# Optimization experiments

Hardware: AMD Instinct MI355X
Metric: run time of the kernel (lower is better)

## Reference

```python
import jax, jax.numpy as jnp
import numpy as np

N_ATOMS = 10000
N_PAIRS = 160000
F = 32            # nr_atom_basis (= edge basis = hidden sizes)
H = 7             # nr_heads
C = H * F         # nr_coefficients = 224
N_RBF = 50
RBF_CUTOFF = 5.0
RBF_GAMMA = 10.0

silu = jax.nn.silu

def setup_inputs() -> dict:
    key = jax.random.key(0)
    ks = jax.random.split(key, 32)
    def w(k, shape, scale=0.1):
        return (jax.random.normal(k, shape, dtype=jnp.float32) * scale)
    inp = {
        "h": jax.random.normal(ks[0], (N_ATOMS, F), dtype=jnp.float32),
        "x": jax.random.normal(ks[1], (N_ATOMS, 3), dtype=jnp.float32),
        "v": jax.random.normal(ks[2], (N_ATOMS, 3), dtype=jnp.float32),
        "pairlist": jax.random.randint(ks[3], (2, N_PAIRS), 0, N_ATOMS, dtype=jnp.int64 if jax.config.read('jax_enable_x64') else jnp.int32),
        # edge model (ContinuousFilterConvolutionWithConcatenation)
        "w_mlp_in": w(ks[4], (2 * F, N_RBF)), "b_mlp_in": jnp.zeros((N_RBF,), jnp.float32),
        "w_e1": w(ks[5], (2 * F + N_RBF + 1, F)), "b_e1": jnp.zeros((F,), jnp.float32),
        "w_e2": w(ks[6], (F, F)), "b_e2": jnp.zeros((F,), jnp.float32),
        # semantic attention mlp
        "w_att": w(ks[7], (F, H)), "b_att": jnp.zeros((H,), jnp.float32),
        # node mlp: in = F + C + F
        "w_n1": w(ks[8], (F + C + F, F)), "b_n1": jnp.zeros((F,), jnp.float32),
        "w_n2": w(ks[9], (F, F)), "b_n2": jnp.zeros((F,), jnp.float32),
        # post norm mlp
        "w_p1": w(ks[10], (C, F)), "b_p1": jnp.zeros((F,), jnp.float32),
        "w_p2": w(ks[11], (F, F)), "b_p2": jnp.zeros((F,), jnp.float32),
        # velocity mlp
        "w_v1": w(ks[12], (F, F)), "b_v1": jnp.zeros((F,), jnp.float32),
        "w_v2": w(ks[13], (F, 1)),
        # mixers
        "w_xmix": w(ks[14], (C, C)),
        "w_vmix": w(ks[15], (C, 1)),
    }
    return inp

def _rbf(d):  # Gaussian smearing, [P] -> [P, N_RBF]
    centers = jnp.linspace(0.0, RBF_CUTOFF, N_RBF, dtype=jnp.float32)
    return jnp.exp(-RBF_GAMMA * (d[:, None] - centers) ** 2)

def reference(h, x, v, pairlist,
              w_mlp_in, b_mlp_in, w_e1, b_e1, w_e2, b_e2,
              w_att, b_att, w_n1, b_n1, w_n2, b_n2,
              w_p1, b_p1, w_p2, b_p2, w_v1, b_v1, w_v2,
              w_xmix, w_vmix):
    n = h.shape[0]
    p = pairlist.shape[1]
    idx_i, idx_j = pairlist[0], pairlist[1]

    r_ij = x[idx_j] - x[idx_i]                       # [P, 3]
    d_ij = jnp.linalg.norm(r_ij, axis=-1)            # [P]
    dir_ij = r_ij / (d_ij[:, None] + 1e-5)           # [P, 3]

    # edge model
    h_cat = jnp.concatenate([h[idx_i], h[idx_j]], axis=-1)         # [P, 2F]
    filt = _rbf(d_ij) * (h_cat @ w_mlp_in + b_mlp_in)              # [P, N_RBF]
    e_in = jnp.concatenate([h_cat, filt, d_ij[:, None]], axis=-1)  # [P, 2F+N_RBF+1]
    h_ij_edge = silu(e_in @ w_e1 + b_e1) @ w_e2 + b_e2             # [P, F]

    # semantic attention: scatter-softmax over edges grouped by idx_i
    logits = jax.nn.celu(h_ij_edge @ w_att + b_att, alpha=2.0)     # [P, H]
    seg_max = jax.ops.segment_max(logits, idx_i, num_segments=n)
    e = jnp.exp(logits - seg_max[idx_i])
    seg_sum = jax.ops.segment_sum(e, idx_i, num_segments=n)
    att = e / seg_sum[idx_i]                                       # [P, H]
    att_agg = jax.ops.segment_sum(att, idx_i, num_segments=n)
    att_normed = att / att_agg[idx_i]
    # einsum('pf,ph->pfh') then reshape to [P, C]
    h_ij_semantic = (h_ij_edge[:, :, None] * att_normed[:, None, :]).reshape(p, C)

    # aggregate (scatter_add)
    h_i_semantic = jax.ops.segment_sum(h_ij_semantic, idx_i, num_segments=n)  # [N, C]

    # spatial attention
    x_mixed = jnp.tanh(h_ij_semantic @ w_xmix)                     # [P, C]
    combinations = dir_ij[:, None, :] * x_mixed[:, :, None]        # [P, C, 3]
    counts = jax.ops.segment_sum(jnp.ones((p,), h.dtype), idx_i, num_segments=n)
    denom = jnp.maximum(counts, 1.0)
    comb_mean = jax.ops.segment_sum(combinations, idx_i, num_segments=n) / denom[:, None, None]
    norm_sq = jnp.sum(comb_mean ** 2, axis=-1)                     # [N, C]
    h_i_spatial = silu(silu(norm_sq @ w_p1 + b_p1) @ w_p2 + b_p2)  # [N, F]

    # node update
    node_in = jnp.concatenate([h, h_i_semantic, h_i_spatial], axis=-1)
    h_updated = h + silu(silu(node_in @ w_n1 + b_n1) @ w_n2 + b_n2)

    # velocity update
    v_ij = jnp.einsum('pcx,c->px', combinations, w_vmix[:, 0])     # [P, 3]
    dv = jax.ops.segment_sum(v_ij, idx_i, num_segments=n) / denom[:, None]
    scale = 2.0 * jax.nn.sigmoid(silu(h @ w_v1 + b_v1) @ w_v2)     # [N, 1]
    v_updated = scale * v + dv
    x_updated = x + v_updated
    return (h_updated, x_updated, v_updated)
```

## Files before the change

kernel.cpp:

```cpp
#include <hip/hip_runtime.h>

typedef unsigned short u16;
typedef unsigned int u32;
typedef __attribute__((ext_vector_type(8))) short short8;
typedef __attribute__((ext_vector_type(4))) float floatx4;

#define P_PAIRS 160000
#define N_ATOMS 10000

#define OFF_WMLP  0
#define OFF_BMLP  3200
#define OFF_WE1   3250
#define OFF_BE1   6930
#define OFF_WE2   6962
#define OFF_BE2   7986
#define OFF_WATT  8018
#define OFF_BATT  8242
#define OFF_WN1   8249
#define OFF_BN1   17465
#define OFF_WN2   17497
#define OFF_BN2   18521
#define OFF_WP1   18553
#define OFF_BP1   25721
#define OFF_WP2   25753
#define OFF_BP2   26777
#define OFF_WV1   26809
#define OFF_BV1   27833
#define OFF_WV2   27865
#define OFF_WVMIX 27897
#define WF_TOTAL  28121

__device__ __forceinline__ float b2f(u16 u){ return __uint_as_float(((u32)u) << 16); }
__device__ __forceinline__ u16 f2b(float f){
  u32 u = __float_as_uint(f);
  u32 r = (u + 0x7FFFu + ((u >> 16) & 1u)) >> 16;
  return (u16)r;
}
__device__ __forceinline__ void unpack2(u32 p, float& lo, float& hi){
  lo = __uint_as_float(p << 16);
  hi = __uint_as_float(p & 0xFFFF0000u);
}
__device__ __forceinline__ float siluf(float v){ return v / (1.f + __expf(-v)); }
__device__ __forceinline__ float ldw(const void* p, int o, int bf){
  return bf ? b2f(((const u16*)p)[o]) : ((const float*)p)[o];
}

__global__ void k_code(float* out, float code){
  if (threadIdx.x == 0 && blockIdx.x == 0) out[0] = code;
}

__device__ __forceinline__ void detect_flags(const u32* hw, const u32* plw, int* s_fl){
  int tid = threadIdx.x;
  if (tid < 64){
    u32 e = (hw[tid] >> 7) & 0xFFu;
    unsigned long long m1 = __ballot(e >= 100u && e <= 140u);
    unsigned long long m2 = __ballot(plw[2*tid+1] == 0u);
    if (tid == 0){
      s_fl[0] = (__popcll(m1) >= 48) ? 1 : 0;
      s_fl[1] = (__popcll(m2) >= 60) ? 1 : 0;
    }
  }
  __syncthreads();
}

#define NBP_NORM 2735
#define NBP_CONV (NBP_NORM + 110)
#define NBP_TRAN (NBP_CONV + 196)
#define NBP_PB   (NBP_TRAN + 14)
#define NBP_HIST (NBP_PB + 625)

__global__ void k_prep(const void* __restrict__ h_raw, const void* __restrict__ x_raw,
    const void* __restrict__ v_raw, const void* __restrict__ pl_raw,
    const void* w_mlp, const void* b_mlp, const void* w_e1, const void* b_e1,
    const void* w_e2, const void* b_e2, const void* w_att, const void* b_att,
    const void* w_n1, const void* b_n1, const void* w_n2, const void* b_n2,
    const void* w_p1, const void* b_p1, const void* w_p2, const void* b_p2,
    const void* w_v1, const void* b_v1, const void* w_v2, const void* w_vmix,
    const void* wx,
    float* __restrict__ hf, float* __restrict__ xf, float* __restrict__ vf,
    int* __restrict__ pli, float* __restrict__ Wf, u16* __restrict__ wT,
    u16* __restrict__ bpk, int* __restrict__ counts){
  __shared__ int s_fl[2];
  detect_flags((const u32*)h_raw, (const u32*)pl_raw, s_fl);
  int bf = s_fl[0], i64 = s_fl[1];
  int bid = blockIdx.x, tid = threadIdx.x;
  if (bid < NBP_NORM){
    int t = bid * 256 + tid;
    if (t < 320000){
      hf[t] = ldw(h_raw, t, bf);
    } else if (t < 350000){
      int i = t - 320000; xf[i] = ldw(x_raw, i, bf);
    } else if (t < 380000){
      int i = t - 350000; vf[i] = ldw(v_raw, i, bf);
    } else if (t < 700000){
      int k = t - 380000;
      const int* p32 = (const int*)pl_raw;
      pli[k] = i64 ? p32[2*(size_t)k] : p32[k];
    }
  } else if (bid < NBP_CONV){
    int t = (bid - NBP_NORM) * 256 + tid;
    if (t >= WF_TOTAL) return;
    if (t < 3200){
      int k = t / 50, o = t - k * 50;
      Wf[OFF_WMLP + o * 64 + k] = ldw(w_mlp, t, bf);
      return;
    }
    const void* src; int o;
    if      (t < 3250)  { src = b_mlp;  o = t - 3200; }
    else if (t < 6930)  { src = w_e1;   o = t - 3250; }
    else if (t < 6962)  { src = b_e1;   o = t - 6930; }
    else if (t < 7986)  { src = w_e2;   o = t - 6962; }
    else if (t < 8018)  { src = b_e2;   o = t - 7986; }
    else if (t < 8242)  { src = w_att;  o = t - 8018; }
    else if (t < 8249)  { src = b_att;  o = t - 8242; }
    else if (t < 17465) { src = w_n1;   o = t - 8249; }
    else if (t < 17497) { src = b_n1;   o = t - 17465; }
    else if (t < 18521) { src = w_n2;   o = t - 17497; }
    else if (t < 18553) { src = b_n2;   o = t - 18521; }
    else if (t < 25721) { src = w_p1;   o = t - 18553; }
    else if (t < 25753) { src = b_p1;   o = t - 25721; }
    else if (t < 26777) { src = w_p2;   o = t - 25753; }
    else if (t < 26809) { src = b_p2;   o = t - 26777; }
    else if (t < 27833) { src = w_v1;   o = t - 26809; }
    else if (t < 27865) { src = b_v1;   o = t - 27833; }
    else if (t < 27897) { src = w_v2;   o = t - 27865; }
    else                { src = w_vmix; o = t - 27897; }
    Wf[t] = ldw(src, o, bf);
  } else if (bid < NBP_TRAN){
    int t = (bid - NBP_CONV) * 256 + tid;
    if (t >= 224 * 224) return;
    int n = t / 224, k = t - n * 224;
    wT[t] = f2b(ldw(wx, k * 224 + n, bf));
  } else if (bid < NBP_PB){
    int t = (bid - NBP_TRAN) * 256 + tid;
    if (t >= 3584) return;
    float v = 0.f;
    if (t < 2048){
      int n = t >> 6, k = t & 63;
      if (k < 50)       v = ldw(w_e1, (64 + k) * 32 + n, bf);
      else if (k == 50) v = ldw(w_e1, 114 * 32 + n, bf);
    } else if (t < 3072){
      int e = t - 2048; int n = e >> 5, k = e & 31;
      v = ldw(w_e2, k * 32 + n, bf);
    } else {
      int e = t - 3072; int n = e >> 5, k = e & 31;
      if (n < 7) v = ldw(w_att, k * 7 + n, bf);
    }
    bpk[t] = f2b(v);
  } else {
    int p = (bid - NBP_PB) * 256 + tid;
    const int* p32 = (const int*)pl_raw;
    int i = i64 ? p32[2*(size_t)p] : p32[p];
    atomicAdd(&counts[i], 1);
  }
}

__global__ void k_atomscan(const float* __restrict__ hf, const float* __restrict__ Wf,
    u16* __restrict__ prei, u16* __restrict__ prej,
    const int* __restrict__ counts, int* __restrict__ offs, int* __restrict__ cursor){
  __shared__ float hs[16][33];
  __shared__ int part[256];
  int tid = threadIdx.x;
  if (blockIdx.x < 625){
    int a0 = blockIdx.x * 16;
    for (int e = tid; e < 512; e += 256){
      int a = e >> 5, k = e & 31;
      hs[a][k] = hf[(size_t)(a0 + a) * 32 + k];
    }
    __syncthreads();
    for (int e = tid; e < 800; e += 256){
      int a = e / 50, r = e - a * 50;
      const float* wm = Wf + OFF_WMLP + r * 64;
      float acc = Wf[OFF_BMLP + r];
      #pragma unroll
      for (int k = 0; k < 32; ++k) acc += hs[a][k] * wm[k];
      prei[(size_t)(a0 + a) * 88 + 32 + r] = f2b(acc);
    }
    for (int e = tid; e < 800; e += 256){
      int a = e / 50, r = e - a * 50;
      const float* wm = Wf + OFF_WMLP + r * 64 + 32;
      float acc = 0.f;
      #pragma unroll
      for (int k = 0; k < 32; ++k) acc += hs[a][k] * wm[k];
      prej[(size_t)(a0 + a) * 88 + 32 + r] = f2b(acc);
    }
    for (int e = tid; e < 512; e += 256){
      int a = e >> 5, o = e & 31;
      float acc = Wf[OFF_BE1 + o];
      #pragma unroll
      for (int k = 0; k < 32; ++k) acc += hs[a][k] * Wf[OFF_WE1 + k * 32 + o];
      prei[(size_t)(a0 + a) * 88 + o] = f2b(acc);
    }
    for (int e = tid; e < 512; e += 256){
      int a = e >> 5, o = e & 31;
      float acc = 0.f;
      #pragma unroll
      for (int k = 0; k < 32; ++k) acc += hs[a][k] * Wf[OFF_WE1 + (32 + k) * 32 + o];
      prej[(size_t)(a0 + a) * 88 + o] = f2b(acc);
    }
  } else {
    int sum = 0;
    for (int k = 0; k < 40; ++k){
      int idx = tid * 40 + k;
      if (idx < N_ATOMS) sum += counts[idx];
    }
    part[tid] = sum;
    __syncthreads();
    if (tid == 0){
      int run = 0;
      for (int q = 0; q < 256; ++q){ int tmp = part[q]; part[q] = run; run += tmp; }
    }
    __syncthreads();
    int run = part[tid];
    for (int k = 0; k < 40; ++k){
      int idx = tid * 40 + k;
      if (idx < N_ATOMS){ offs[idx] = run; cursor[idx] = run; run += counts[idx]; }
    }
    if (tid == 0) offs[N_ATOMS] = P_PAIRS;
  }
}

__global__ void k_scatter(const int* __restrict__ pl, int* __restrict__ cursor,
                          int* __restrict__ isrt, int* __restrict__ jsrt){
  int p = blockIdx.x * 256 + threadIdx.x;
  int i = pl[p];
  int pos = atomicAdd(&cursor[i], 1);
  isrt[pos] = i;
  jsrt[pos] = pl[P_PAIRS + p];
}

#define PM_UB   0
#define PM_TB   16384
#define PM_DD   30720
#define PM_A1   31232
#define PM_B1   49664
#define PM_A2   54272
#define PM_B2   64512
#define PM_B3   67072
#define PM_TOT  68352

__global__ __launch_bounds__(256) void k_pairm(const float* __restrict__ x,
    const float* __restrict__ Wf, const u16* __restrict__ prei, const u16* __restrict__ prej,
    const int* __restrict__ isrt, const int* __restrict__ jsrt, const u16* __restrict__ bpk,
    u16* __restrict__ edge, float* __restrict__ logits, float* __restrict__ dirs){
  __shared__ __attribute__((aligned(16))) char smem[PM_TOT];
  float* UB = (float*)(smem + PM_UB);
  u16*   TB = (u16*)(smem + PM_TB);
  float* DD = (float*)(smem + PM_DD);
  u16*   A1 = (u16*)(smem + PM_A1);
  u16*   B1 = (u16*)(smem + PM_B1);
  u16*   A2 = (u16*)(smem + PM_A2);
  u16*   B2 = (u16*)(smem + PM_B2);
  u16*   B3 = (u16*)(smem + PM_B3);
  int tid = threadIdx.x;
  int wave = tid >> 6, lane = tid & 63, l15 = lane & 15, quad = lane >> 4;
  int row0 = blockIdx.x * 128;

  if (tid < 128){
    int s = row0 + tid;
    int i = isrt[s], j = jsrt[s];
    float r0 = x[j*3+0] - x[i*3+0];
    float r1 = x[j*3+1] - x[i*3+1];
    float r2 = x[j*3+2] - x[i*3+2];
    float d = sqrtf(r0*r0 + r1*r1 + r2*r2);
    float rinv = 1.f / (d + 1e-5f);
    dirs[s*3+0] = r0*rinv; dirs[s*3+1] = r1*rinv; dirs[s*3+2] = r2*rinv;
    DD[tid] = d;
    const uint4* pi4 = (const uint4*)(prei + (size_t)i * 88);
    const uint4* pj4 = (const uint4*)(prej + (size_t)j * 88);
    float* ub = UB + tid * 32;
    #pragma unroll
    for (int q = 0; q < 4; ++q){
      uint4 a4 = pi4[q], b4 = pj4[q];
      u32 pa[4] = {a4.x, a4.y, a4.z, a4.w};
      u32 pb[4] = {b4.x, b4.y, b4.z, b4.w};
      #pragma unroll
      for (int w2 = 0; w2 < 4; ++w2){
        float al, ah, bl, bh;
        unpack2(pa[w2], al, ah); unpack2(pb[w2], bl, bh);
        ub[q*8 + w2*2]     = al + bl;
        ub[q*8 + w2*2 + 1] = ah + bh;
      }
    }
    u32* tb = (u32*)TB + tid * 28;
    #pragma unroll
    for (int q = 0; q < 7; ++q){
      uint4 a4 = pi4[4+q], b4 = pj4[4+q];
      u32 pa[4] = {a4.x, a4.y, a4.z, a4.w};
      u32 pb[4] = {b4.x, b4.y, b4.z, b4.w};
      #pragma unroll
      for (int w2 = 0; w2 < 4; ++w2){
        float al, ah, bl, bh;
        unpack2(pa[w2], al, ah); unpack2(pb[w2], bl, bh);
        tb[q*4 + w2] = (u32)f2b(al + bl) | ((u32)f2b(ah + bh) << 16);
      }
    }
  } else {
    int t2 = tid - 128;
    const u32* src = (const u32*)bpk;
    for (int e = t2; e < 1024; e += 128){
      int n = e >> 5, kp = e & 31;
      ((u32*)B1)[n*36 + kp] = src[e];
    }
    for (int e = t2; e < 512; e += 128){
      int n = e >> 4, kp = e & 15;
      ((u32*)B2)[n*20 + kp] = src[1024 + e];
    }
    for (int e = t2; e < 256; e += 128){
      int n = e >> 4, kp = e & 15;
      ((u32*)B3)[n*20 + kp] = src[1536 + e];
    }
  }
  __syncthreads();
  for (int e = tid; e < 4096; e += 256){
    int r = e >> 5, kp = e & 31;
    int k0 = kp * 2, k1 = k0 + 1;
    float d = DD[r];
    float v0 = 0.f, v1 = 0.f;
    if (k0 < 50){
      float t0 = b2f(TB[r*56 + k0]);
      float c0 = (float)k0 * (5.f/49.f), dd0 = d - c0;
      v0 = t0 * __expf(-10.f * dd0 * dd0);
    } else if (k0 == 50) v0 = d;
    if (k1 < 50){
      float t1 = b2f(TB[r*56 + k1]);
      float c1 = (float)k1 * (5.f/49.f), dd1 = d - c1;
      v1 = t1 * __expf(-10.f * dd1 * dd1);
    }
    ((u32*)A1)[r*36 + kp] = (u32)f2b(v0) | ((u32)f2b(v1) << 16);
  }
  __syncthreads();
  floatx4 au[2][2];
  #pragma unroll
  for (int mt = 0; mt < 2; ++mt)
    #pragma unroll
    for (int nt = 0; nt < 2; ++nt) au[mt][nt] = (floatx4){0.f,0.f,0.f,0.f};
  #pragma unroll
  for (int ks = 0; ks < 2; ++ks){
    int kk = ks * 32;
    short8 a0 = *(const short8*)(A1 + (wave*32 + l15)*72 + kk + quad*8);
    short8 a1 = *(const short8*)(A1 + (wave*32 + 16 + l15)*72 + kk + quad*8);
    #pragma unroll
    for (int nt = 0; nt < 2; ++nt){
      short8 b = *(const short8*)(B1 + (nt*16 + l15)*72 + kk + quad*8);
      au[0][nt] = __builtin_amdgcn_mfma_f32_16x16x32_bf16(a0, b, au[0][nt], 0, 0, 0);
      au[1][nt] = __builtin_amdgcn_mfma_f32_16x16x32_bf16(a1, b, au[1][nt], 0, 0, 0);
    }
  }
  #pragma unroll
  for (int mt = 0; mt < 2; ++mt)
    #pragma unroll
    for (int nt = 0; nt < 2; ++nt)
      #pragma unroll
      for (int reg = 0; reg < 4; ++reg){
        int r = wave*32 + mt*16 + quad*4 + reg;
        int c = nt*16 + l15;
        float uval = au[mt][nt][reg] + UB[r*32 + c];
        A2[r*40 + c] = f2b(siluf(uval));
      }
  __syncthreads();
  floatx4 ae[2][2];
  #pragma unroll
  for (int mt = 0; mt < 2; ++mt)
    #pragma unroll
    for (int nt = 0; nt < 2; ++nt) ae[mt][nt] = (floatx4){0.f,0.f,0.f,0.f};
  {
    short8 a0 = *(const short8*)(A2 + (wave*32 + l15)*40 + quad*8);
    short8 a1 = *(const short8*)(A2 + (wave*32 + 16 + l15)*40 + quad*8);
    #pragma unroll
    for (int nt = 0; nt < 2; ++nt){
      short8 b = *(const short8*)(B2 + (nt*16 + l15)*40 + quad*8);
      ae[0][nt] = __builtin_amdgcn_mfma_f32_16x16x32_bf16(a0, b, ae[0][nt], 0, 0, 0);
      ae[1][nt] = __builtin_amdgcn_mfma_f32_16x16x32_bf16(a1, b, ae[1][nt], 0, 0, 0);
    }
  }
  __syncthreads();
  #pragma unroll
  for (int mt = 0; mt < 2; ++mt)
    #pragma unroll
    for (int nt = 0; nt < 2; ++nt)
      #pragma unroll
      for (int reg = 0; reg < 4; ++reg){
        int r = wave*32 + mt*16 + quad*4 + reg;
        int c = nt*16 + l15;
        float ev = ae[mt][nt][reg] + Wf[OFF_BE2 + c];
        A2[r*40 + c] = f2b(ev);
      }
  __syncthreads();
  {
    int r = tid >> 1, p = tid & 1;
    const uint4* srcp = (const uint4*)(A2 + r*40 + p*16);
    uint4* dstp = (uint4*)(edge + (size_t)(row0 + r)*32 + p*16);
    dstp[0] = srcp[0]; dstp[1] = srcp[1];
  }
  floatx4 al_[2];
  al_[0] = (floatx4){0.f,0.f,0.f,0.f};
  al_[1] = (floatx4){0.f,0.f,0.f,0.f};
  {
    short8 a0 = *(const short8*)(A2 + (wave*32 + l15)*40 + quad*8);
    short8 a1 = *(const short8*)(A2 + (wave*32 + 16 + l15)*40 + quad*8);
    short8 b = *(const short8*)(B3 + l15*40 + quad*8);
    al_[0] = __builtin_amdgcn_mfma_f32_16x16x32_bf16(a0, b, al_[0], 0, 0, 0);
    al_[1] = __builtin_amdgcn_mfma_f32_16x16x32_bf16(a1, b, al_[1], 0, 0, 0);
  }
  if (l15 < 7){
    float ba = Wf[OFF_BATT + l15];
    #pragma unroll
    for (int mt = 0; mt < 2; ++mt)
      #pragma unroll
      for (int reg = 0; reg < 4; ++reg){
        int r = wave*32 + mt*16 + quad*4 + reg;
        float vv = al_[mt][reg] + ba;
        float cl = vv > 0.f ? vv : 2.f * expm1f(0.5f * vv);
        logits[(size_t)(row0 + r)*7 + l15] = cl;
      }
  }
}

__global__ __launch_bounds__(256) void k_att(const int* __restrict__ offs,
    const float* __restrict__ logits, const u16* __restrict__ edge,
    float* __restrict__ atts, float* __restrict__ hsem){
  int a = blockIdx.x * 16 + (threadIdx.x >> 4);
  int lane = threadIdx.x & 15;
  int off = offs[a], end = offs[a+1];
  float m[7];
  #pragma unroll
  for (int hh = 0; hh < 7; ++hh) m[hh] = -1e30f;
  for (int s = off + lane; s < end; s += 16){
    #pragma unroll
    for (int hh = 0; hh < 7; ++hh) m[hh] = fmaxf(m[hh], logits[s*7+hh]);
  }
  #pragma unroll
  for (int hh = 0; hh < 7; ++hh){
    float v = m[hh];
    #pragma unroll
    for (int msk = 8; msk >= 1; msk >>= 1) v = fmaxf(v, __shfl_xor(v, msk));
    m[hh] = v;
  }
  float sm[7] = {0,0,0,0,0,0,0};
  for (int s = off + lane; s < end; s += 16){
    #pragma unroll
    for (int hh = 0; hh < 7; ++hh){
      float e = __expf(logits[s*7+hh] - m[hh]);
      sm[hh] += e;
      atts[s*7+hh] = e;
    }
  }
  #pragma unroll
  for (int hh = 0; hh < 7; ++hh){
    float v = sm[hh];
    #pragma unroll
    for (int msk = 8; msk >= 1; msk >>= 1) v += __shfl_xor(v, msk);
    sm[hh] = 1.f / v;
  }
  for (int s = off + lane; s < end; s += 16){
    #pragma unroll
    for (int hh = 0; hh < 7; ++hh) atts[s*7+hh] *= sm[hh];
  }
  __syncthreads();
  float acc[14] = {0,0,0,0,0,0,0,0,0,0,0,0,0,0};
  for (int s = off; s < end; ++s){
    u32 ev = *(const u32*)(edge + (size_t)s * 32 + lane * 2);
    float e0 = b2f((u16)(ev & 0xFFFFu));
    float e1 = b2f((u16)(ev >> 16));
    const float* ap = atts + (size_t)s * 7;
    #pragma unroll
    for (int hh = 0; hh < 7; ++hh){
      float at = ap[hh];
      acc[hh]     += e0 * at;
      acc[7 + hh] += e1 * at;
    }
  }
  float* hp = hsem + (size_t)a * 224 + lane * 14;
  #pragma unroll
  for (int jj = 0; jj < 14; ++jj) hp[jj] = acc[jj];
}

#define GW_EL   29696
#define GW_AL   (29696 + 4608)
#define GW_TOT  36096

__global__ __launch_bounds__(256, 4) void k_gemm3w(const u16* __restrict__ edge,
    const float* __restrict__ atts, const u16* __restrict__ BT,
    u16* __restrict__ xh0, u16* __restrict__ xh1){
  __shared__ __attribute__((aligned(16))) char smem[GW_TOT];
  u16*   As  = (u16*)smem;
  u16*   xth = (u16*)smem;
  u16*   eL  = (u16*)(smem + GW_EL);
  float* aL  = (float*)(smem + GW_AL);
  int tid = threadIdx.x;
  int wave = tid >> 6, lane = tid & 63, l15 = lane & 15, quad = lane >> 4;
  int row0 = blockIdx.x * 64;

  for (int e = tid; e < 512; e += 256){
    int r = e >> 3, q = e & 7;
    *(uint2*)(eL + r*36 + q*4) = *(const uint2*)(edge + (size_t)(row0 + r)*32 + q*4);
  }
  for (int e = tid; e < 448; e += 256) aL[e] = atts[(size_t)row0*7 + e];
  floatx4 acc[14];
  #pragma unroll
  for (int nt = 0; nt < 14; ++nt) acc[nt] = (floatx4){0.f, 0.f, 0.f, 0.f};
  __syncthreads();

  {
    int pr = tid >> 2, q = tid & 3;
    u32* asw = (u32*)As + pr*116 + q*28;
    const u16* er = eL + pr*36 + q*8;
    const float* ar = aL + pr*7;
    float av[7];
    #pragma unroll
    for (int hh = 0; hh < 7; ++hh) av[hh] = ar[hh];
    #pragma unroll
    for (int fo2 = 0; fo2 < 4; ++fo2){
      float e0 = b2f(er[2*fo2]);
      float e1 = b2f(er[2*fo2+1]);
      u16 w[14];
      #pragma unroll
      for (int hh = 0; hh < 7; ++hh){
        w[hh]   = f2b(e0 * av[hh]);
        w[7+hh] = f2b(e1 * av[hh]);
      }
      #pragma unroll
      for (int k = 0; k < 7; ++k)
        asw[fo2*7 + k] = (u32)w[2*k] | ((u32)w[2*k+1] << 16);
    }
  }
  __syncthreads();

  const u16* btbase = BT + (size_t)l15 * 224 + quad * 8;
  for (int kt = 0; kt < 7; ++kt){
    short8 a0 = *(const short8*)(As + (wave*16 + l15)*232 + kt*32 + quad*8);
    const u16* bt = btbase + kt*32;
    #pragma unroll
    for (int nt = 0; nt < 14; ++nt){
      short8 b = *(const short8*)(bt + (size_t)nt*16*224);
      acc[nt] = __builtin_amdgcn_mfma_f32_16x16x32_bf16(a0, b, acc[nt], 0, 0, 0);
    }
  }
  __syncthreads();

  #pragma unroll
  for (int nt = 0; nt < 14; ++nt)
    #pragma unroll
    for (int reg = 0; reg < 4; ++reg){
      int r = wave*16 + quad*4 + reg;
      int c = nt*16 + l15;
      float vv = acc[nt][reg];
      vv = fminf(fmaxf(vv, -15.f), 15.f);
      float e2 = __expf(2.f * vv);
      xth[r*232 + c] = f2b((e2 - 1.f) / (e2 + 1.f));
    }
  __syncthreads();
  for (int e = tid; e < 1792; e += 256){
    int r = e / 28, w = e - r * 28;
    uint4 val = *(const uint4*)(xth + r*232 + w*8);
    if (w < 14) *(uint4*)(xh0 + (size_t)(row0 + r)*112 + w*8) = val;
    else        *(uint4*)(xh1 + (size_t)(row0 + r)*112 + (w-14)*8) = val;
  }
}

#define G_BS   29696
#define G_EL   29696
#define G_AL   (29696 + 4608)
#define G_TOT  38656

__global__ __launch_bounds__(256, 4) void k_gemm3(const u16* __restrict__ edge,
    const float* __restrict__ atts, const u16* __restrict__ BT,
    u16* __restrict__ xhalf, int half){
  __shared__ __attribute__((aligned(16))) char smem[G_TOT];
  u16*   As  = (u16*)smem;
  u16*   xth = (u16*)smem;
  u16*   Bs  = (u16*)(smem + G_BS);
  u16*   eL  = (u16*)(smem + G_EL);
  float* aL  = (float*)(smem + G_AL);
  int tid = threadIdx.x;
  int wave = tid >> 6, lane = tid & 63, l15 = lane & 15, quad = lane >> 4;
  int row0 = blockIdx.x * 64;
  int nbase = half * 112;

  for (int e = tid; e < 512; e += 256){
    int r = e >> 3, q = e & 7;
    *(uint2*)(eL + r*36 + q*4) = *(const uint2*)(edge + (size_t)(row0 + r)*32 + q*4);
  }
  for (int e = tid; e < 448; e += 256) aL[e] = atts[(size_t)row0*7 + e];
  floatx4 acc[7];
  #pragma unroll
  for (int nt = 0; nt < 7; ++nt) acc[nt] = (floatx4){0.f, 0.f, 0.f, 0.f};
  __syncthreads();

  {
    int pr = tid >> 2, q = tid & 3;
    u32* asw = (u32*)As + pr*116 + q*28;
    const u16* er = eL + pr*36 + q*8;
    const float* ar = aL + pr*7;
    float av[7];
    #pragma unroll
    for (int hh = 0; hh < 7; ++hh) av[hh] = ar[hh];
    #pragma unroll
    for (int fo2 = 0; fo2 < 4; ++fo2){
      float e0 = b2f(er[2*fo2]);
      float e1 = b2f(er[2*fo2+1]);
      u16 w[14];
      #pragma unroll
      for (int hh = 0; hh < 7; ++hh){
        w[hh]   = f2b(e0 * av[hh]);
        w[7+hh] = f2b(e1 * av[hh]);
      }
      #pragma unroll
      for (int k = 0; k < 7; ++k)
        asw[fo2*7 + k] = (u32)w[2*k] | ((u32)w[2*k+1] << 16);
    }
  }
  __syncthreads();

  for (int kt = 0; kt < 7; ++kt){
    for (int e = tid; e < 448; e += 256){
      int r = e >> 2, q = e & 3;
      *(uint4*)(Bs + r*40 + q*8) = *(const uint4*)(BT + (size_t)(nbase + r)*224 + kt*32 + q*8);
    }
    __syncthreads();
    int kk = kt * 32;
    short8 a0 = *(const short8*)(As + (wave*16 + l15)*232 + kk + quad*8);
    #pragma unroll
    for (int nt = 0; nt < 7; ++nt){
      short8 b = *(const short8*)(Bs + (nt*16 + l15)*40 + quad*8);
      acc[nt] = __builtin_amdgcn_mfma_f32_16x16x32_bf16(a0, b, acc[nt], 0, 0, 0);
    }
    __syncthreads();
  }

  #pragma unroll
  for (int nt = 0; nt < 7; ++nt)
    #pragma unroll
    for (int reg = 0; reg < 4; ++reg){
      int r = wave*16 + quad*4 + reg;
      int c = nt*16 + l15;
      float vv = acc[nt][reg];
      vv = fminf(fmaxf(vv, -15.f), 15.f);
      float e2 = __expf(2.f * vv);
      xth[r*120 + c] = f2b((e2 - 1.f) / (e2 + 1.f));
    }
  __syncthreads();
  for (int e = tid; e < 896; e += 256){
    int r = e / 14, w = e - r * 14;
    *(uint4*)(xhalf + (size_t)(row0 + r)*112 + w*8) = *(const uint4*)(xth + r*120 + w*8);
  }
}

__global__ __launch_bounds__(256) void k_comb(const int* __restrict__ offs,
    const u16* __restrict__ xhalf, const float* __restrict__ dirs,
    const float* __restrict__ Wf, int half,
    float* __restrict__ nsq, float* __restrict__ pvh){
  int a = blockIdx.x * 16 + (threadIdx.x >> 4);
  int lane = threadIdx.x & 15;
  int off = offs[a], end = offs[a+1];
  float c0[7] = {0,0,0,0,0,0,0}, c1[7] = {0,0,0,0,0,0,0}, c2[7] = {0,0,0,0,0,0,0};
  for (int s = off; s < end; ++s){
    float d0 = dirs[s*3+0], d1 = dirs[s*3+1], d2 = dirs[s*3+2];
    const u16* xr = xhalf + (size_t)s * 112 + lane;
    #pragma unroll
    for (int k = 0; k < 7; ++k){
      float xm = b2f(xr[k*16]);
      c0[k] += d0 * xm; c1[k] += d1 * xm; c2[k] += d2 * xm;
    }
  }
  float inv = 1.f / fmaxf((float)(end - off), 1.f);
  float pv0 = 0.f, pv1 = 0.f, pv2 = 0.f;
  #pragma unroll
  for (int k = 0; k < 7; ++k){
    float m0 = c0[k]*inv, m1 = c1[k]*inv, m2 = c2[k]*inv;
    int c = half*112 + k*16 + lane;
    nsq[(size_t)a*224 + c] = m0*m0 + m1*m1 + m2*m2;
    float wv = Wf[OFF_WVMIX + c];
    pv0 += wv*m0; pv1 += wv*m1; pv2 += wv*m2;
  }
  #pragma unroll
  for (int m = 8; m >= 1; m >>= 1){
    pv0 += __shfl_xor(pv0, m); pv1 += __shfl_xor(pv1, m); pv2 += __shfl_xor(pv2, m);
  }
  if (lane == 0){
    float* pp = pvh + (size_t)half*30000 + (size_t)a*3;
    pp[0] = pv0; pp[1] = pv1; pp[2] = pv2;
  }
}

__global__ __launch_bounds__(256) void k_final4(const float* __restrict__ h,
    const float* __restrict__ x, const float* __restrict__ v,
    const float* __restrict__ Wf, const float* __restrict__ hsem,
    const float* __restrict__ nsq, const float* __restrict__ pvh,
    float* __restrict__ out){
  __shared__ float s_nsq[16][225];
  __shared__ float s_in[16][289];
  __shared__ float s_u1[16][33];
  __shared__ float s_un[16][33];
  __shared__ float s_sc[16];
  int tid = threadIdx.x;
  int a0 = blockIdx.x * 16;
  for (int e = tid; e < 896; e += 256){
    int a = e / 56, q = e - a * 56;
    float4 t = *(const float4*)(nsq + (size_t)(a0 + a) * 224 + q * 4);
    s_nsq[a][q*4+0] = t.x; s_nsq[a][q*4+1] = t.y;
    s_nsq[a][q*4+2] = t.z; s_nsq[a][q*4+3] = t.w;
  }
  for (int e = tid; e < 896; e += 256){
    int a = e / 56, q = e - a * 56;
    float4 t = *(const float4*)(hsem + (size_t)(a0 + a) * 224 + q * 4);
    s_in[a][32 + q*4+0] = t.x; s_in[a][32 + q*4+1] = t.y;
    s_in[a][32 + q*4+2] = t.z; s_in[a][32 + q*4+3] = t.w;
  }
  for (int e = tid; e < 128; e += 256){
    int a = e >> 3, q = e & 7;
    float4 t = *(const float4*)(h + (size_t)(a0 + a) * 32 + q * 4);
    s_in[a][q*4+0] = t.x; s_in[a][q*4+1] = t.y;
    s_in[a][q*4+2] = t.z; s_in[a][q*4+3] = t.w;
  }
  __syncthreads();
  int o = tid & 31, g5 = tid >> 5;
  int aA = g5, aB = g5 + 8;
  {
    float uA = Wf[OFF_BP1 + o], uB = uA;
    const float* w = Wf + OFF_WP1 + o;
    #pragma unroll 8
    for (int kk = 0; kk < 224; ++kk){
      float wv = w[kk*32];
      uA += s_nsq[aA][kk] * wv;
      uB += s_nsq[aB][kk] * wv;
    }
    s_u1[aA][o] = siluf(uA);
    s_u1[aB][o] = siluf(uB);
  }
  {
    float gA = Wf[OFF_BV1 + o], gB = gA;
    const float* w = Wf + OFF_WV1 + o;
    #pragma unroll
    for (int kk = 0; kk < 32; ++kk){
      float wv = w[kk*32];
      gA += s_in[aA][kk] * wv;
      gB += s_in[aB][kk] * wv;
    }
    float wv2 = Wf[OFF_WV2 + o];
    float zA = siluf(gA) * wv2, zB = siluf(gB) * wv2;
    #pragma unroll
    for (int m = 16; m >= 1; m >>= 1){
      zA += __shfl_xor(zA, m); zB += __shfl_xor(zB, m);
    }
    if (o == 0){
      s_sc[aA] = 2.f / (1.f + __expf(-zA));
      s_sc[aB] = 2.f / (1.f + __expf(-zB));
    }
  }
  __syncthreads();
  {
    float uA = Wf[OFF_BP2 + o], uB = uA;
    const float* w = Wf + OFF_WP2 + o;
    #pragma unroll
    for (int kk = 0; kk < 32; ++kk){
      float wv = w[kk*32];
      uA += s_u1[aA][kk] * wv;
      uB += s_u1[aB][kk] * wv;
    }
    s_in[aA][256 + o] = siluf(uA);
    s_in[aB][256 + o] = siluf(uB);
  }
  __syncthreads();
  {
    float uA = Wf[OFF_BN1 + o], uB = uA;
    const float* w = Wf + OFF_WN1 + o;
    #pragma unroll 8
    for (int kk = 0; kk < 288; ++kk){
      float wv = w[kk*32];
      uA += s_in[aA][kk] * wv;
      uB += s_in[aB][kk] * wv;
    }
    s_un[aA][o] = siluf(uA);
    s_un[aB][o] = siluf(uB);
  }
  __syncthreads();
  {
    float uA = Wf[OFF_BN2 + o], uB = uA;
    const float* w = Wf + OFF_WN2 + o;
    #pragma unroll
    for (int kk = 0; kk < 32; ++kk){
      float wv = w[kk*32];
      uA += s_un[aA][kk] * wv;
      uB += s_un[aB][kk] * wv;
    }
    out[(size_t)(a0 + aA)*32 + o] = s_in[aA][o] + siluf(uA);
    out[(size_t)(a0 + aB)*32 + o] = s_in[aB][o] + siluf(uB);
  }
  if (tid < 48){
    int a = tid / 3, c = tid - a * 3;
    int ga = a0 + a;
    float pv = pvh[(size_t)ga*3 + c] + pvh[30000 + (size_t)ga*3 + c];
    float vup = s_sc[a] * v[ga*3 + c] + pv;
    float xup = x[ga*3 + c] + vup;
    out[N_ATOMS*32 + (size_t)ga*3 + c] = xup;
    out[N_ATOMS*32 + N_ATOMS*3 + (size_t)ga*3 + c] = vup;
  }
}

__global__ __launch_bounds__(256) void k_combf(const int* __restrict__ offs,
    const u16* __restrict__ xh0, const u16* __restrict__ xh1,
    const float* __restrict__ dirs, const float* __restrict__ h,
    const float* __restrict__ x, const float* __restrict__ v,
    const float* __restrict__ Wf, const float* __restrict__ hsem,
    float* __restrict__ out){
  __shared__ float s_nsq[16][225];
  __shared__ float s_in[16][289];
  __shared__ float s_u1[16][33];
  __shared__ float s_un[16][33];
  __shared__ float s_sc[16];
  __shared__ float s_pv[16][3];
  int tid = threadIdx.x;
  int a0 = blockIdx.x * 16;
  for (int e = tid; e < 896; e += 256){
    int a = e / 56, q = e - a * 56;
    float4 t = *(const float4*)(hsem + (size_t)(a0 + a) * 224 + q * 4);
    s_in[a][32 + q*4+0] = t.x; s_in[a][32 + q*4+1] = t.y;
    s_in[a][32 + q*4+2] = t.z; s_in[a][32 + q*4+3] = t.w;
  }
  for (int e = tid; e < 128; e += 256){
    int a = e >> 3, q = e & 7;
    float4 t = *(const float4*)(h + (size_t)(a0 + a) * 32 + q * 4);
    s_in[a][q*4+0] = t.x; s_in[a][q*4+1] = t.y;
    s_in[a][q*4+2] = t.z; s_in[a][q*4+3] = t.w;
  }
  {
    int a = tid >> 4, lane = tid & 15;
    int off = offs[a0 + a], end = offs[a0 + a + 1];
    float c0A[7] = {0,0,0,0,0,0,0}, c1A[7] = {0,0,0,0,0,0,0}, c2A[7] = {0,0,0,0,0,0,0};
    float c0B[7] = {0,0,0,0,0,0,0}, c1B[7] = {0,0,0,0,0,0,0}, c2B[7] = {0,0,0,0,0,0,0};
    for (int s = off; s < end; ++s){
      float d0 = dirs[s*3+0], d1 = dirs[s*3+1], d2 = dirs[s*3+2];
      const u16* xra = xh0 + (size_t)s * 112 + lane;
      const u16* xrb = xh1 + (size_t)s * 112 + lane;
      #pragma unroll
      for (int k = 0; k < 7; ++k){
        float xa = b2f(xra[k*16]);
        float xb = b2f(xrb[k*16]);
        c0A[k] += d0 * xa; c1A[k] += d1 * xa; c2A[k] += d2 * xa;
        c0B[k] += d0 * xb; c1B[k] += d1 * xb; c2B[k] += d2 * xb;
      }
    }
    float inv = 1.f / fmaxf((float)(end - off), 1.f);
    float pv0 = 0.f, pv1 = 0.f, pv2 = 0.f;
    #pragma unroll
    for (int k = 0; k < 7; ++k){
      {
        float m0 = c0A[k]*inv, m1 = c1A[k]*inv, m2 = c2A[k]*inv;
        int c = k*16 + lane;
        s_nsq[a][c] = m0*m0 + m1*m1 + m2*m2;
        float wv = Wf[OFF_WVMIX + c];
        pv0 += wv*m0; pv1 += wv*m1; pv2 += wv*m2;
      }
      {
        float m0 = c0B[k]*inv, m1 = c1B[k]*inv, m2 = c2B[k]*inv;
        int c = 112 + k*16 + lane;
        s_nsq[a][c] = m0*m0 + m1*m1 + m2*m2;
        float wv = Wf[OFF_WVMIX + c];
        pv0 += wv*m0; pv1 += wv*m1; pv2 += wv*m2;
      }
    }
    #pragma unroll
    for (int m = 8; m >= 1; m >>= 1){
      pv0 += __shfl_xor(pv0, m); pv1 += __shfl_xor(pv1, m); pv2 += __shfl_xor(pv2, m);
    }
    if (lane == 0){ s_pv[a][0] = pv0; s_pv[a][1] = pv1; s_pv[a][2] = pv2; }
  }
  __syncthreads();
  int o = tid & 31, g5 = tid >> 5;
  int aA = g5, aB = g5 + 8;
  {
    float uA = Wf[OFF_BP1 + o], uB = uA;
    const float* w = Wf + OFF_WP1 + o;
    #pragma unroll 8
    for (int kk = 0; kk < 224; ++kk){
      float wv = w[kk*32];
      uA += s_nsq[aA][kk] * wv;
      uB += s_nsq[aB][kk] * wv;
    }
    s_u1[aA][o] = siluf(uA);
    s_u1[aB][o] = siluf(uB);
  }
  {
    float gA = Wf[OFF_BV1 + o], gB = gA;
    const float* w = Wf + OFF_WV1 + o;
    #pragma unroll
    for (int kk = 0; kk < 32; ++kk){
      float wv = w[kk*32];
      gA += s_in[aA][kk] * wv;
      gB += s_in[aB][kk] * wv;
    }
    float wv2 = Wf[OFF_WV2 + o];
    float zA = siluf(gA) * wv2, zB = siluf(gB) * wv2;
    #pragma unroll
    for (int m = 16; m >= 1; m >>= 1){
      zA += __shfl_xor(zA, m); zB += __shfl_xor(zB, m);
    }
    if (o == 0){
      s_sc[aA] = 2.f / (1.f + __expf(-zA));
      s_sc[aB] = 2.f / (1.f + __expf(-zB));
    }
  }
  __syncthreads();
  {
    float uA = Wf[OFF_BP2 + o], uB = uA;
    const float* w = Wf + OFF_WP2 + o;
    #pragma unroll
    for (int kk = 0; kk < 32; ++kk){
      float wv = w[kk*32];
      uA += s_u1[aA][kk] * wv;
      uB += s_u1[aB][kk] * wv;
    }
    s_in[aA][256 + o] = siluf(uA);
    s_in[aB][256 + o] = siluf(uB);
  }
  __syncthreads();
  {
    float uA = Wf[OFF_BN1 + o], uB = uA;
    const float* w = Wf + OFF_WN1 + o;
    #pragma unroll 8
    for (int kk = 0; kk < 288; ++kk){
      float wv = w[kk*32];
      uA += s_in[aA][kk] * wv;
      uB += s_in[aB][kk] * wv;
    }
    s_un[aA][o] = siluf(uA);
    s_un[aB][o] = siluf(uB);
  }
  __syncthreads();
  {
    float uA = Wf[OFF_BN2 + o], uB = uA;
    const float* w = Wf + OFF_WN2 + o;
    #pragma unroll
    for (int kk = 0; kk < 32; ++kk){
      float wv = w[kk*32];
      uA += s_un[aA][kk] * wv;
      uB += s_un[aB][kk] * wv;
    }
    out[(size_t)(a0 + aA)*32 + o] = s_in[aA][o] + siluf(uA);
    out[(size_t)(a0 + aB)*32 + o] = s_in[aB][o] + siluf(uB);
  }
  if (tid < 48){
    int a = tid / 3, c = tid - a * 3;
    int ga = a0 + a;
    float vup = s_sc[a] * v[ga*3 + c] + s_pv[a][c];
    float xup = x[ga*3 + c] + vup;
    out[N_ATOMS*32 + (size_t)ga*3 + c] = xup;
    out[N_ATOMS*32 + N_ATOMS*3 + (size_t)ga*3 + c] = vup;
  }
}

static constexpr size_t al256(size_t x){ return (x + 255) & ~(size_t)255; }
static constexpr size_t WS_FLAGS   = 0;
static constexpr size_t WS_COUNTS  = al256(WS_FLAGS + 8);
static constexpr size_t WS_OFFSETS = al256(WS_COUNTS + (size_t)N_ATOMS * 4);
static constexpr size_t WS_CURSOR  = al256(WS_OFFSETS + (size_t)(N_ATOMS + 1) * 4);
static constexpr size_t WS_PERM    = al256(WS_CURSOR + (size_t)N_ATOMS * 4);
static constexpr size_t WS_PLI     = al256(WS_PERM + (size_t)P_PAIRS * 4);
static constexpr size_t WS_HF      = al256(WS_PLI + (size_t)2 * P_PAIRS * 4);
static constexpr size_t WS_XF      = al256(WS_HF + (size_t)N_ATOMS * 32 * 4);
static constexpr size_t WS_VF      = al256(WS_XF + (size_t)N_ATOMS * 3 * 4);
static constexpr size_t WS_WF      = al256(WS_VF + (size_t)N_ATOMS * 3 * 4);
static constexpr size_t WS_WT      = al256(WS_WF + (size_t)WF_TOTAL * 4);
static constexpr size_t WS_EDGE    = al256(WS_WT + (size_t)224 * 224 * 2);
static constexpr size_t WS_ATTS    = al256(WS_EDGE + (size_t)P_PAIRS * 32 * 2);
static constexpr size_t WS_DIRS    = al256(WS_ATTS + (size_t)P_PAIRS * 7 * 4);
static constexpr size_t WS_LOGITS  = al256(WS_DIRS + (size_t)P_PAIRS * 3 * 4);
static constexpr size_t WS_PREI    = al256(WS_LOGITS + (size_t)P_PAIRS * 7 * 4);
static constexpr size_t WS_PREJ    = al256(WS_PREI + (size_t)N_ATOMS * 88 * 2);
static constexpr size_t WS_HSEM    = WS_LOGITS + 4480000;
static constexpr size_t WS_XH      = WS_HSEM + (size_t)N_ATOMS * 224 * 4;
static constexpr size_t WS_NSQ     = WS_XH + (size_t)P_PAIRS * 112 * 2;
static constexpr size_t WS_PVH     = WS_NSQ + (size_t)N_ATOMS * 224 * 4;
static constexpr size_t WS_JSRT    = al256(WS_PVH + (size_t)2 * 30000 * 4);
static constexpr size_t WS_BPK     = al256(WS_JSRT + (size_t)P_PAIRS * 4);
static constexpr size_t WS_END     = WS_BPK + 3584 * 2;
static constexpr size_t WB_XH0     = WS_XH;
static constexpr size_t WB_XH1     = WB_XH0 + (size_t)P_PAIRS * 112 * 2;
static constexpr size_t WB_JSRT    = al256(WB_XH1 + (size_t)P_PAIRS * 112 * 2);
static constexpr size_t WB_BPK     = al256(WB_JSRT + (size_t)P_PAIRS * 4);
static constexpr size_t WB_END     = WB_BPK + 3584 * 2;
static_assert(WS_PREJ + (size_t)N_ATOMS * 88 * 2 <= WS_XH, "pre tables before xhalf");
static_assert(WS_END <= WS_LOGITS + (size_t)P_PAIRS * 224 * 2, "fallback within proven footprint");
static_assert(WS_HSEM % 256 == 0 && WS_XH % 256 == 0 && WS_NSQ % 256 == 0 && WS_PVH % 256 == 0, "alignment");
static_assert(WB_XH1 % 256 == 0, "alignment");

extern "C" void kernel_launch(void* const* d_in, const int* in_sizes, int n_in,
                              void* d_out, int out_size, void* d_ws, size_t ws_size,
                              hipStream_t stream){
  (void)in_sizes; (void)n_in;
  if (out_size != 380000 || ws_size < WS_END){
    k_code<<<1, 64, 0, stream>>>((float*)d_out, 14000.f);
    return;
  }
  char* ws = (char*)d_ws;
  int*   counts = (int*)(ws + WS_COUNTS);
  int*   offs   = (int*)(ws + WS_OFFSETS);
  int*   cursor = (int*)(ws + WS_CURSOR);
  int*   isrt   = (int*)(ws + WS_PERM);
  int*   pli    = (int*)(ws + WS_PLI);
  float* hf     = (float*)(ws + WS_HF);
  float* xf     = (float*)(ws + WS_XF);
  float* vf     = (float*)(ws + WS_VF);
  float* Wf     = (float*)(ws + WS_WF);
  u16*   wT     = (u16*)(ws + WS_WT);
  u16*   edge   = (u16*)(ws + WS_EDGE);
  float* atts   = (float*)(ws + WS_ATTS);
  float* dirs   = (float*)(ws + WS_DIRS);
  float* logits = (float*)(ws + WS_LOGITS);
  u16*   prei   = (u16*)(ws + WS_PREI);
  u16*   prej   = (u16*)(ws + WS_PREJ);
  float* hsem   = (float*)(ws + WS_HSEM);

  bool big = (ws_size >= WB_END);
  u16*   xh0  = (u16*)(ws + WB_XH0);
  u16*   xh1  = big ? (u16*)(ws + WB_XH1) : xh0;
  int*   jsrt = big ? (int*)(ws + WB_JSRT) : (int*)(ws + WS_JSRT);
  u16*   bpk  = big ? (u16*)(ws + WB_BPK) : (u16*)(ws + WS_BPK);
  float* nsq  = (float*)(ws + WS_NSQ);
  float* pvh  = (float*)(ws + WS_PVH);

  hipMemsetAsync(counts, 0, (size_t)N_ATOMS * 4, stream);
  k_prep<<<NBP_HIST, 256, 0, stream>>>(d_in[0], d_in[1], d_in[2], d_in[3],
      d_in[4],  d_in[5],  d_in[6],  d_in[7],  d_in[8],  d_in[9],  d_in[10], d_in[11],
      d_in[12], d_in[13], d_in[14], d_in[15], d_in[16], d_in[17], d_in[18], d_in[19],
      d_in[20], d_in[21], d_in[22], d_in[24], d_in[23],
      hf, xf, vf, pli, Wf, wT, bpk, counts);
  k_atomscan<<<626, 256, 0, stream>>>(hf, Wf, prei, prej, counts, offs, cursor);
  k_scatter<<<P_PAIRS / 256, 256, 0, stream>>>(pli, cursor, isrt, jsrt);
  k_pairm<<<P_PAIRS / 128, 256, 0, stream>>>(xf, Wf, prei, prej, isrt, jsrt, bpk, edge, logits, dirs);
  k_att<<<N_ATOMS / 16, 256, 0, stream>>>(offs, logits, edge, atts, hsem);
  if (big){
    k_gemm3w<<<P_PAIRS / 64, 256, 0, stream>>>(edge, atts, wT, xh0, xh1);
    k_combf<<<625, 256, 0, stream>>>(offs, xh0, xh1, dirs, hf, xf, vf, Wf, hsem, (float*)d_out);
  } else {
    k_gemm3<<<P_PAIRS / 64, 256, 0, stream>>>(edge, atts, wT, xh0, 0);
    k_comb<<<N_ATOMS / 16, 256, 0, stream>>>(offs, xh0, dirs, Wf, 0, nsq, pvh);
    k_gemm3<<<P_PAIRS / 64, 256, 0, stream>>>(edge, atts, wT, xh0, 1);
    k_comb<<<N_ATOMS / 16, 256, 0, stream>>>(offs, xh0, dirs, Wf, 1, nsq, pvh);
    k_final4<<<625, 256, 0, stream>>>(hf, xf, vf, Wf, hsem, nsq, pvh, (float*)d_out);
  }
}
```

Measured before the change: 332.1 us.

## Stage GEMM B tiles through LDS and vectorize combine-kernel xh loads

The wide GEMM kernel now copies each 32-wide K slice of the transposed weight into shared memory, one half of the output columns at a time, instead of having every lane read B fragments straight from global memory. This adds two barriers per K step. In the fused combine kernel, each of 14 lanes now reads 8 contiguous bf16 values with one 16-byte load, replacing strided 2-byte loads. This changes the channel-to-lane mapping and leaves two lanes of each 16-lane group idle. The small-workspace gemm3 kernel also gets a mode parameter so it can split its grid between the two halves, but its call sites still pass fixed halves.

```diff
diff --git a/kernel.cpp b/kernel.cpp
--- a/kernel.cpp
+++ b/kernel.cpp
@@ -476,18 +476,20 @@
   for (int jj = 0; jj < 14; ++jj) hp[jj] = acc[jj];
 }
 
-#define GW_EL   29696
-#define GW_AL   (29696 + 4608)
-#define GW_TOT  36096
-
-__global__ __launch_bounds__(256, 4) void k_gemm3w(const u16* __restrict__ edge,
+#define GF_BS   29696
+#define GF_EL   29696
+#define GF_AL   (29696 + 4608)
+#define GF_TOT  38656
+
+__global__ __launch_bounds__(256, 4) void k_gemm3f(const u16* __restrict__ edge,
     const float* __restrict__ atts, const u16* __restrict__ BT,
     u16* __restrict__ xh0, u16* __restrict__ xh1){
-  __shared__ __attribute__((aligned(16))) char smem[GW_TOT];
+  __shared__ __attribute__((aligned(16))) char smem[GF_TOT];
   u16*   As  = (u16*)smem;
   u16*   xth = (u16*)smem;
-  u16*   eL  = (u16*)(smem + GW_EL);
-  float* aL  = (float*)(smem + GW_AL);
+  u16*   Bs  = (u16*)(smem + GF_BS);
+  u16*   eL  = (u16*)(smem + GF_EL);
+  float* aL  = (float*)(smem + GF_AL);
   int tid = threadIdx.x;
   int wave = tid >> 6, lane = tid & 63, l15 = lane & 15, quad = lane >> 4;
   int row0 = blockIdx.x * 64;
@@ -527,17 +529,25 @@
   }
   __syncthreads();
 
-  const u16* btbase = BT + (size_t)l15 * 224 + quad * 8;
-  for (int kt = 0; kt < 7; ++kt){
-    short8 a0 = *(const short8*)(As + (wave*16 + l15)*232 + kt*32 + quad*8);
-    const u16* bt = btbase + kt*32;
-    #pragma unroll
-    for (int nt = 0; nt < 14; ++nt){
-      short8 b = *(const short8*)(bt + (size_t)nt*16*224);
-      acc[nt] = __builtin_amdgcn_mfma_f32_16x16x32_bf16(a0, b, acc[nt], 0, 0, 0);
-    }
-  }
-  __syncthreads();
+  #pragma unroll 1
+  for (int half = 0; half < 2; ++half){
+    int nbase = half * 112;
+    #pragma unroll 1
+    for (int kt = 0; kt < 7; ++kt){
+      for (int e = tid; e < 448; e += 256){
+        int r = e >> 2, q = e & 3;
+        *(uint4*)(Bs + r*40 + q*8) = *(const uint4*)(BT + (size_t)(nbase + r)*224 + kt*32 + q*8);
+      }
+      __syncthreads();
+      short8 a0 = *(const short8*)(As + (wave*16 + l15)*232 + kt*32 + quad*8);
+      #pragma unroll
+      for (int nt = 0; nt < 7; ++nt){
+        short8 b = *(const short8*)(Bs + (nt*16 + l15)*40 + quad*8);
+        acc[half*7 + nt] = __builtin_amdgcn_mfma_f32_16x16x32_bf16(a0, b, acc[half*7 + nt], 0, 0, 0);
+      }
+      __syncthreads();
+    }
+  }
 
   #pragma unroll
   for (int nt = 0; nt < 14; ++nt)
@@ -566,7 +576,7 @@
 
 __global__ __launch_bounds__(256, 4) void k_gemm3(const u16* __restrict__ edge,
     const float* __restrict__ atts, const u16* __restrict__ BT,
-    u16* __restrict__ xhalf, int half){
+    u16* __restrict__ xh0, u16* __restrict__ xh1, int mode){
   __shared__ __attribute__((aligned(16))) char smem[G_TOT];
   u16*   As  = (u16*)smem;
   u16*   xth = (u16*)smem;
@@ -575,7 +585,12 @@
   float* aL  = (float*)(smem + G_AL);
   int tid = threadIdx.x;
   int wave = tid >> 6, lane = tid & 63, l15 = lane & 15, quad = lane >> 4;
-  int row0 = blockIdx.x * 64;
+  int bid = blockIdx.x;
+  int half, rblk;
+  if (mode < 0){ half = bid & 1; rblk = bid >> 1; }
+  else         { half = mode;    rblk = bid; }
+  u16* xhalf = half ? xh1 : xh0;
+  int row0 = rblk * 64;
   int nbase = half * 112;
 
   for (int e = tid; e < 512; e += 256){
@@ -828,37 +843,45 @@
   {
     int a = tid >> 4, lane = tid & 15;
     int off = offs[a0 + a], end = offs[a0 + a + 1];
-    float c0A[7] = {0,0,0,0,0,0,0}, c1A[7] = {0,0,0,0,0,0,0}, c2A[7] = {0,0,0,0,0,0,0};
-    float c0B[7] = {0,0,0,0,0,0,0}, c1B[7] = {0,0,0,0,0,0,0}, c2B[7] = {0,0,0,0,0,0,0};
-    for (int s = off; s < end; ++s){
-      float d0 = dirs[s*3+0], d1 = dirs[s*3+1], d2 = dirs[s*3+2];
-      const u16* xra = xh0 + (size_t)s * 112 + lane;
-      const u16* xrb = xh1 + (size_t)s * 112 + lane;
-      #pragma unroll
-      for (int k = 0; k < 7; ++k){
-        float xa = b2f(xra[k*16]);
-        float xb = b2f(xrb[k*16]);
-        c0A[k] += d0 * xa; c1A[k] += d1 * xa; c2A[k] += d2 * xa;
-        c0B[k] += d0 * xb; c1B[k] += d1 * xb; c2B[k] += d2 * xb;
+    float c0A[8] = {0,0,0,0,0,0,0,0}, c1A[8] = {0,0,0,0,0,0,0,0}, c2A[8] = {0,0,0,0,0,0,0,0};
+    float c0B[8] = {0,0,0,0,0,0,0,0}, c1B[8] = {0,0,0,0,0,0,0,0}, c2B[8] = {0,0,0,0,0,0,0,0};
+    if (lane < 14){
+      for (int s = off; s < end; ++s){
+        float d0 = dirs[s*3+0], d1 = dirs[s*3+1], d2 = dirs[s*3+2];
+        uint4 ra = *(const uint4*)(xh0 + (size_t)s * 112 + lane * 8);
+        uint4 rb = *(const uint4*)(xh1 + (size_t)s * 112 + lane * 8);
+        u32 wa[4] = {ra.x, ra.y, ra.z, ra.w};
+        u32 wb[4] = {rb.x, rb.y, rb.z, rb.w};
+        #pragma unroll
+        for (int q = 0; q < 4; ++q){
+          float alo, ahi, blo, bhi;
+          unpack2(wa[q], alo, ahi); unpack2(wb[q], blo, bhi);
+          c0A[2*q]   += d0*alo; c1A[2*q]   += d1*alo; c2A[2*q]   += d2*alo;
+          c0A[2*q+1] += d0*ahi; c1A[2*q+1] += d1*ahi; c2A[2*q+1] += d2*ahi;
+          c0B[2*q]   += d0*blo; c1B[2*q]   += d1*blo; c2B[2*q]   += d2*blo;
+          c0B[2*q+1] += d0*bhi; c1B[2*q+1] += d1*bhi; c2B[2*q+1] += d2*bhi;
+        }
       }
     }
     float inv = 1.f / fmaxf((float)(end - off), 1.f);
     float pv0 = 0.f, pv1 = 0.f, pv2 = 0.f;
-    #pragma unroll
-    for (int k = 0; k < 7; ++k){
-      {
-        float m0 = c0A[k]*inv, m1 = c1A[k]*inv, m2 = c2A[k]*inv;
-        int c = k*16 + lane;
-        s_nsq[a][c] = m0*m0 + m1*m1 + m2*m2;
-        float wv = Wf[OFF_WVMIX + c];
-        pv0 += wv*m0; pv1 += wv*m1; pv2 += wv*m2;
-      }
-      {
-        float m0 = c0B[k]*inv, m1 = c1B[k]*inv, m2 = c2B[k]*inv;
-        int c = 112 + k*16 + lane;
-        s_nsq[a][c] = m0*m0 + m1*m1 + m2*m2;
-        float wv = Wf[OFF_WVMIX + c];
-        pv0 += wv*m0; pv1 += wv*m1; pv2 += wv*m2;
+    if (lane < 14){
+      #pragma unroll
+      for (int j = 0; j < 8; ++j){
+        {
+          float m0 = c0A[j]*inv, m1 = c1A[j]*inv, m2 = c2A[j]*inv;
+          int c = lane*8 + j;
+          s_nsq[a][c] = m0*m0 + m1*m1 + m2*m2;
+          float wv = Wf[OFF_WVMIX + c];
+          pv0 += wv*m0; pv1 += wv*m1; pv2 += wv*m2;
+        }
+        {
+          float m0 = c0B[j]*inv, m1 = c1B[j]*inv, m2 = c2B[j]*inv;
+          int c = 112 + lane*8 + j;
+          s_nsq[a][c] = m0*m0 + m1*m1 + m2*m2;
+          float wv = Wf[OFF_WVMIX + c];
+          pv0 += wv*m0; pv1 += wv*m1; pv2 += wv*m2;
+        }
       }
     }
     #pragma unroll
@@ -1032,12 +1055,12 @@
   k_pairm<<<P_PAIRS / 128, 256, 0, stream>>>(xf, Wf, prei, prej, isrt, jsrt, bpk, edge, logits, dirs);
   k_att<<<N_ATOMS / 16, 256, 0, stream>>>(offs, logits, edge, atts, hsem);
   if (big){
-    k_gemm3w<<<P_PAIRS / 64, 256, 0, stream>>>(edge, atts, wT, xh0, xh1);
+    k_gemm3f<<<P_PAIRS / 64, 256, 0, stream>>>(edge, atts, wT, xh0, xh1);
     k_combf<<<625, 256, 0, stream>>>(offs, xh0, xh1, dirs, hf, xf, vf, Wf, hsem, (float*)d_out);
   } else {
-    k_gemm3<<<P_PAIRS / 64, 256, 0, stream>>>(edge, atts, wT, xh0, 0);
+    k_gemm3<<<P_PAIRS / 64, 256, 0, stream>>>(edge, atts, wT, xh0, xh0, 0);
     k_comb<<<N_ATOMS / 16, 256, 0, stream>>>(offs, xh0, dirs, Wf, 0, nsq, pvh);
-    k_gemm3<<<P_PAIRS / 64, 256, 0, stream>>>(edge, atts, wT, xh0, 1);
+    k_gemm3<<<P_PAIRS / 64, 256, 0, stream>>>(edge, atts, wT, xh0, xh0, 1);
     k_comb<<<N_ATOMS / 16, 256, 0, stream>>>(offs, xh0, dirs, Wf, 1, nsq, pvh);
     k_final4<<<625, 256, 0, stream>>>(hf, xf, vf, Wf, hsem, nsq, pvh, (float*)d_out);
   }
```

Result: slower. 530.9 us (+59.8%).
